# Kernel optimization log

Measured on AMD Instinct MI355X. Metric: run time of the kernel, lower is better.

Reference implementation:

```python
import jax, jax.numpy as jnp
import numpy as np

D_MODEL = 1024
N_HEADS = 16
D_K = D_MODEL // N_HEADS


def setup_inputs() -> dict:
    key = jax.random.key(0)
    ks = jax.random.split(key, 5)
    x = jax.random.normal(ks[0], (4, 2048, D_MODEL), dtype=jnp.float32)
    # nn.Linear stores weight as [out, in]; we store transposed [in, out] for x @ W
    w_qkv = jax.random.normal(ks[1], (D_MODEL, 3 * D_MODEL), dtype=jnp.float32) / np.sqrt(D_MODEL)
    b_qkv = jnp.zeros((3 * D_MODEL,), dtype=jnp.float32)
    w_fc = jax.random.normal(ks[2], (D_MODEL, D_MODEL), dtype=jnp.float32) / np.sqrt(D_MODEL)
    b_fc = jnp.zeros((D_MODEL,), dtype=jnp.float32)
    ln_g = jnp.ones((D_MODEL,), dtype=jnp.float32)
    ln_b = jnp.zeros((D_MODEL,), dtype=jnp.float32)
    return {"x": x, "w_qkv": w_qkv, "b_qkv": b_qkv, "w_fc": w_fc, "b_fc": b_fc,
            "ln_g": ln_g, "ln_b": ln_b}


def _layernorm(x, g, b, eps=1e-5):
    mu = jnp.mean(x, axis=-1, keepdims=True)
    var = jnp.mean(jnp.square(x - mu), axis=-1, keepdims=True)
    return (x - mu) * jax.lax.rsqrt(var + eps) * g + b


def reference(x, w_qkv, b_qkv, w_fc, b_fc, ln_g, ln_b):
    residual = x
    xn = _layernorm(x, ln_g, ln_b)
    B, L, D = xn.shape
    qkv = xn @ w_qkv + b_qkv  # [B, L, 3D]
    q, k, v = jnp.split(qkv, 3, axis=-1)
    # b l (h d) -> b h l d
    def to_heads(t):
        return t.reshape(B, L, N_HEADS, D_K).transpose(0, 2, 1, 3)
    q, k, v = to_heads(q), to_heads(k), to_heads(v)
    scale = 1.0 / np.sqrt(D_K)
    scores = jnp.einsum('bhld,bhmd->bhlm', q, k) * scale  # [B,H,L,L]
    attn = jax.nn.softmax(scores, axis=-1)
    # dropout is identity in eval mode
    out = jnp.einsum('bhlm,bhmd->bhld', attn, v)  # [B,H,L,d]
    out = out.transpose(0, 2, 1, 3).reshape(B, L, D)  # b h l d -> b l (h d)
    out = out @ w_fc + b_fc
    return out + residual
```

## Files before the change

kernel.cpp:

```cpp
#include <hip/hip_runtime.h>
#include <hip/hip_bf16.h>
#include <cstdint>
#include <cstddef>

using bf16 = __hip_bfloat16;
typedef __attribute__((ext_vector_type(4))) float f32x4;
typedef __attribute__((ext_vector_type(8))) short bf16x8;

#define D_MODEL 1024
#define SEQ     2048
#define NB      4
#define NHEAD   16
#define DHEAD   64
#define NROWS   (NB * SEQ)

__device__ __forceinline__ void load_lds16(const void* g, void* l) {
  __builtin_amdgcn_global_load_lds(
      (const __attribute__((address_space(1))) unsigned int*)g,
      (__attribute__((address_space(3))) unsigned int*)l, 16, 0, 0);
}

__device__ __forceinline__ unsigned short f2bf(float f) {
  bf16 h = __float2bfloat16(f);
  return *(unsigned short*)&h;
}

__device__ __forceinline__ unsigned pk_trunc(float a, float b) {
  union { float f; unsigned u; } ca, cb;
  ca.f = a; cb.f = b;
  return (ca.u >> 16) | (cb.u & 0xffff0000u);
}

__global__ __launch_bounds__(256) void prep_kernel(
    const float* __restrict__ x, const float* __restrict__ g,
    const float* __restrict__ bb, bf16* __restrict__ xn,
    const float* __restrict__ w_qkv, bf16* __restrict__ wqkvT,
    const float* __restrict__ w_fc, bf16* __restrict__ wfcT) {
  __shared__ float tile[32][33];
  if (blockIdx.x < 2048) {
    int row  = blockIdx.x * 4 + (threadIdx.x >> 6);
    int lane = threadIdx.x & 63;
    const float4* xr = (const float4*)(x + (size_t)row * D_MODEL);
    float v[16], s = 0.f;
#pragma unroll
    for (int i = 0; i < 4; i++) {
      float4 t = xr[lane + 64 * i];
      v[4 * i] = t.x; v[4 * i + 1] = t.y; v[4 * i + 2] = t.z; v[4 * i + 3] = t.w;
      s += t.x + t.y + t.z + t.w;
    }
#pragma unroll
    for (int off = 32; off; off >>= 1) s += __shfl_xor(s, off, 64);
    float mean = s * (1.f / D_MODEL);
    float vs = 0.f;
#pragma unroll
    for (int i = 0; i < 16; i++) { float d = v[i] - mean; vs += d * d; }
#pragma unroll
    for (int off = 32; off; off >>= 1) vs += __shfl_xor(vs, off, 64);
    float rstd = rsqrtf(vs * (1.f / D_MODEL) + 1e-5f);
    ushort4* op = (ushort4*)(xn + (size_t)row * D_MODEL);
#pragma unroll
    for (int i = 0; i < 4; i++) {
      float4 gv = ((const float4*)g)[lane + 64 * i];
      float4 bv = ((const float4*)bb)[lane + 64 * i];
      ushort4 o;
      o.x = f2bf((v[4 * i]     - mean) * rstd * gv.x + bv.x);
      o.y = f2bf((v[4 * i + 1] - mean) * rstd * gv.y + bv.y);
      o.z = f2bf((v[4 * i + 2] - mean) * rstd * gv.z + bv.z);
      o.w = f2bf((v[4 * i + 3] - mean) * rstd * gv.w + bv.w);
      op[lane + 64 * i] = o;
    }
  } else {
    int b2 = blockIdx.x - 2048;
    int bx = b2 & 127, by = b2 >> 7;
    const float* in; bf16* out; int C, c0;
    if (bx < 96) { in = w_qkv; out = wqkvT; C = 3072; c0 = bx * 32; }
    else         { in = w_fc;  out = wfcT;  C = 1024; c0 = (bx - 96) * 32; }
    int r0 = by * 32;
    int tx = threadIdx.x & 31, ty = threadIdx.x >> 5;
    for (int i = ty; i < 32; i += 8)
      tile[i][tx] = in[(size_t)(r0 + i) * C + c0 + tx];
    __syncthreads();
    for (int i = ty; i < 32; i += 8)
      out[(size_t)(c0 + i) * 1024 + r0 + tx] = __float2bfloat16(tile[tx][i]);
  }
}

__device__ __forceinline__ void store_ct(bf16* p, float v)  { *p = __float2bfloat16(v); }
__device__ __forceinline__ void store_ct(float* p, float v) { *p = v; }

template <int SPLIT, int RESID, typename CT>
__global__ __launch_bounds__(256) void gemm_bt(
    const bf16* __restrict__ A, const bf16* __restrict__ Bt,
    const float* __restrict__ bias, const float* __restrict__ resid,
    CT* __restrict__ C, bf16* __restrict__ vt, int M, int N, int K) {
  __shared__ __attribute__((aligned(16))) bf16 Alds[128 * 64];
  __shared__ __attribute__((aligned(16))) bf16 Blds[128 * 64];
  int tid = threadIdx.x, wave = tid >> 6, lane = tid & 63;
  int ntiles = N >> 7;
  int bm = blockIdx.x / ntiles, bn = blockIdx.x % ntiles;
  int m0 = bm << 7, n0 = bn << 7;
  int wm = (wave >> 1) << 6, wn = (wave & 1) << 6;
  int srow = tid >> 3;
  int sw8  = (((tid & 7) ^ (srow & 7)) << 3);
  int frow = lane & 15, quad = lane >> 4;
  const bf16* Ap[4];
  const bf16* Bp[4];
#pragma unroll
  for (int s = 0; s < 4; s++) {
    Ap[s] = A  + (size_t)(m0 + s * 32 + srow) * K + sw8;
    Bp[s] = Bt + (size_t)(n0 + s * 32 + srow) * K + sw8;
  }
  f32x4 acc[4][4] = {};
  for (int k0 = 0; k0 < K; k0 += 64) {
    __syncthreads();
#pragma unroll
    for (int s = 0; s < 4; s++) {
      load_lds16(Ap[s], (char*)Alds + s * 4096 + tid * 16);
      load_lds16(Bp[s], (char*)Blds + s * 4096 + tid * 16);
      Ap[s] += 64; Bp[s] += 64;
    }
    __syncthreads();
    bf16x8 af[4][2], bv[4][2];
#pragma unroll
    for (int i = 0; i < 4; i++)
#pragma unroll
      for (int kk = 0; kk < 2; kk++) {
        int e = (((kk * 4 + quad) ^ (frow & 7)) << 3);
        af[i][kk] = *(const bf16x8*)&Alds[(wm + i * 16 + frow) * 64 + e];
        bv[i][kk] = *(const bf16x8*)&Blds[(wn + i * 16 + frow) * 64 + e];
      }
#pragma unroll
    for (int i = 0; i < 4; i++)
#pragma unroll
      for (int j = 0; j < 4; j++) {
        acc[i][j] = __builtin_amdgcn_mfma_f32_16x16x32_bf16(af[i][0], bv[j][0], acc[i][j], 0, 0, 0);
        acc[i][j] = __builtin_amdgcn_mfma_f32_16x16x32_bf16(af[i][1], bv[j][1], acc[i][j], 0, 0, 0);
      }
  }
#pragma unroll
  for (int i = 0; i < 4; i++) {
    int row0 = m0 + wm + i * 16 + (quad << 2);
#pragma unroll
    for (int j = 0; j < 4; j++) {
      int col = n0 + wn + j * 16 + frow;
      float bvs = bias[col];
      if (SPLIT && col >= 2048) {
        int hd = col - 2048;
        int b = row0 >> 11, seq0 = row0 & 2047;
        int within = seq0 & 63, mt = within >> 4, q4 = (within >> 2) & 3;
        int pos = (seq0 & ~63) + ((mt >> 1) << 5) + (q4 << 3) + ((mt & 1) << 2);
        ushort4 pk;
        pk.x = f2bf(acc[i][j][0] + bvs);
        pk.y = f2bf(acc[i][j][1] + bvs);
        pk.z = f2bf(acc[i][j][2] + bvs);
        pk.w = f2bf(acc[i][j][3] + bvs);
        *(ushort4*)&vt[((size_t)(b * 1024 + hd)) * SEQ + pos] = pk;
      } else {
        int stride = SPLIT ? 2048 : N;
        float scale = (SPLIT && col < 1024) ? 0.18033688f : 1.0f;
#pragma unroll
        for (int r = 0; r < 4; r++) {
          size_t idx = (size_t)(row0 + r) * stride + col;
          float val = (acc[i][j][r] + bvs) * scale;
          if (RESID) val += resid[idx];
          store_ct(&C[idx], val);
        }
      }
    }
  }
}

__global__ __launch_bounds__(256) void gemm_fc64(
    const bf16* __restrict__ A, const bf16* __restrict__ Bt,
    const float* __restrict__ bias, const float* __restrict__ resid,
    float* __restrict__ out) {
  __shared__ __attribute__((aligned(16))) bf16 Alds[128 * 64];
  __shared__ __attribute__((aligned(16))) bf16 Blds[64 * 64];
  int tid = threadIdx.x, wave = tid >> 6, lane = tid & 63;
  int bm = blockIdx.x >> 4, bn = blockIdx.x & 15;
  int m0 = bm << 7, n0 = bn << 6;
  int wm = (wave >> 1) << 6, wn = (wave & 1) << 5;
  int srow = tid >> 3;
  int sw8  = (((tid & 7) ^ (srow & 7)) << 3);
  int frow = lane & 15, quad = lane >> 4;
  const bf16* Ap[4];
  const bf16* Bp[2];
#pragma unroll
  for (int s = 0; s < 4; s++)
    Ap[s] = A + (size_t)(m0 + s * 32 + srow) * 1024 + sw8;
#pragma unroll
  for (int s = 0; s < 2; s++)
    Bp[s] = Bt + (size_t)(n0 + s * 32 + srow) * 1024 + sw8;
  f32x4 acc[4][2] = {};
  for (int k0 = 0; k0 < 1024; k0 += 64) {
    __syncthreads();
#pragma unroll
    for (int s = 0; s < 4; s++) {
      load_lds16(Ap[s], (char*)Alds + s * 4096 + tid * 16);
      Ap[s] += 64;
    }
#pragma unroll
    for (int s = 0; s < 2; s++) {
      load_lds16(Bp[s], (char*)Blds + s * 4096 + tid * 16);
      Bp[s] += 64;
    }
    __syncthreads();
    bf16x8 af[4][2], bv[2][2];
#pragma unroll
    for (int kk = 0; kk < 2; kk++) {
      int e = (((kk * 4 + quad) ^ (frow & 7)) << 3);
#pragma unroll
      for (int i = 0; i < 4; i++)
        af[i][kk] = *(const bf16x8*)&Alds[(wm + i * 16 + frow) * 64 + e];
#pragma unroll
      for (int j = 0; j < 2; j++)
        bv[j][kk] = *(const bf16x8*)&Blds[(wn + j * 16 + frow) * 64 + e];
    }
#pragma unroll
    for (int i = 0; i < 4; i++)
#pragma unroll
      for (int j = 0; j < 2; j++) {
        acc[i][j] = __builtin_amdgcn_mfma_f32_16x16x32_bf16(af[i][0], bv[j][0], acc[i][j], 0, 0, 0);
        acc[i][j] = __builtin_amdgcn_mfma_f32_16x16x32_bf16(af[i][1], bv[j][1], acc[i][j], 0, 0, 0);
      }
  }
#pragma unroll
  for (int i = 0; i < 4; i++) {
    int row0 = m0 + wm + i * 16 + (quad << 2);
#pragma unroll
    for (int j = 0; j < 2; j++) {
      int col = n0 + wn + j * 16 + frow;
      float bvs = bias[col];
#pragma unroll
      for (int r = 0; r < 4; r++) {
        size_t idx = (size_t)(row0 + r) * 1024 + col;
        out[idx] = (acc[i][j][r] + bvs) + resid[idx];
      }
    }
  }
}


__device__ __forceinline__ void stage_kv(
    const bf16* Kp0, const bf16* Kp1, const bf16* Vp0, const bf16* Vp1,
    bf16* KB, bf16* VB, int tid) {
  load_lds16(Kp0, (char*)KB + tid * 16);
  load_lds16(Kp1, (char*)KB + 4096 + tid * 16);
  load_lds16(Vp0, (char*)VB + tid * 16);
  load_lds16(Vp1, (char*)VB + 4096 + tid * 16);
}

__device__ __forceinline__ void kv_tile(
    const bf16* KL, const bf16* VL, int frow, int e0,
    const bf16x8 (&qf)[2][2], f32x4 (&l4)[2], f32x4 (&o)[4][2]) {
  f32x4 s[4][2] = {};
#pragma unroll
  for (int mt = 0; mt < 4; mt++) {
    bf16x8 af0 = *(const bf16x8*)&KL[(mt * 16 + frow) * 64 + e0];
    bf16x8 af1 = *(const bf16x8*)&KL[(mt * 16 + frow) * 64 + (e0 ^ 32)];
#pragma unroll
    for (int qt2 = 0; qt2 < 2; qt2++) {
      s[mt][qt2] = __builtin_amdgcn_mfma_f32_16x16x32_bf16(af0, qf[qt2][0], s[mt][qt2], 0, 0, 0);
      s[mt][qt2] = __builtin_amdgcn_mfma_f32_16x16x32_bf16(af1, qf[qt2][1], s[mt][qt2], 0, 0, 0);
    }
  }
  uint2 pk[2][4];
#pragma unroll
  for (int qt2 = 0; qt2 < 2; qt2++)
#pragma unroll
    for (int mt = 0; mt < 4; mt++) {
      f32x4 pv;
      pv[0] = __builtin_amdgcn_exp2f(s[mt][qt2][0]);
      pv[1] = __builtin_amdgcn_exp2f(s[mt][qt2][1]);
      pv[2] = __builtin_amdgcn_exp2f(s[mt][qt2][2]);
      pv[3] = __builtin_amdgcn_exp2f(s[mt][qt2][3]);
      l4[qt2] += pv;
      pk[qt2][mt].x = pk_trunc(pv[0], pv[1]);
      pk[qt2][mt].y = pk_trunc(pv[2], pv[3]);
    }
#pragma unroll
  for (int dt = 0; dt < 4; dt++) {
    bf16x8 vf0 = *(const bf16x8*)&VL[(dt * 16 + frow) * 64 + e0];
    bf16x8 vf1 = *(const bf16x8*)&VL[(dt * 16 + frow) * 64 + (e0 ^ 32)];
#pragma unroll
    for (int qt2 = 0; qt2 < 2; qt2++) {
      union { unsigned u[4]; bf16x8 v; } pf0, pf1;
      pf0.u[0] = pk[qt2][0].x; pf0.u[1] = pk[qt2][0].y;
      pf0.u[2] = pk[qt2][1].x; pf0.u[3] = pk[qt2][1].y;
      pf1.u[0] = pk[qt2][2].x; pf1.u[1] = pk[qt2][2].y;
      pf1.u[2] = pk[qt2][3].x; pf1.u[3] = pk[qt2][3].y;
      o[dt][qt2] = __builtin_amdgcn_mfma_f32_16x16x32_bf16(vf0, pf0.v, o[dt][qt2], 0, 0, 0);
      o[dt][qt2] = __builtin_amdgcn_mfma_f32_16x16x32_bf16(vf1, pf1.v, o[dt][qt2], 0, 0, 0);
    }
  }
}

__global__ __launch_bounds__(256, 4) void attn_kernel(
    const bf16* __restrict__ qk, const bf16* __restrict__ vt,
    bf16* __restrict__ aout) {
  int bh = blockIdx.x;
  int qt = blockIdx.y;
  int bb = bh >> 4, h = bh & 15;
  const bf16* Qg = qk + (size_t)bb * SEQ * 2048 + h * DHEAD;
  const bf16* Kg = Qg + D_MODEL;
  const bf16* Vg = vt + (size_t)bh * DHEAD * SEQ;

  __shared__ __attribute__((aligned(16))) bf16 Qlds[128 * 64];
  __shared__ __attribute__((aligned(16))) bf16 Klds[64 * 64];
  __shared__ __attribute__((aligned(16))) bf16 Vlds[64 * 64];

  int tid = threadIdx.x, wave = tid >> 6, lane = tid & 63;
  int prow = tid >> 3, pch = tid & 7;
  int lch8 = ((pch ^ (prow & 7)) << 3);
  int frow = lane & 15, quad = lane >> 4;
  int e0 = ((quad ^ (frow & 7)) << 3);
  int q0 = qt * 128;

  bf16* K0 = Klds;  bf16* V0 = Vlds;
  bf16* K1 = Qlds;  bf16* V1 = Qlds + 64 * 64;

  const bf16* Kp0 = Kg + (size_t)prow * 2048 + lch8;
  const bf16* Kp1 = Kg + (size_t)(32 + prow) * 2048 + lch8;
  const bf16* Vp0 = Vg + (size_t)prow * SEQ + lch8;
  const bf16* Vp1 = Vg + (size_t)(32 + prow) * SEQ + lch8;
  const size_t KT = (size_t)1 << 17;

#pragma unroll
  for (int s2 = 0; s2 < 4; s2++)
    load_lds16(Qg + (size_t)(q0 + s2 * 32 + prow) * 2048 + lch8,
               (char*)Qlds + s2 * 4096 + tid * 16);
  __syncthreads();
  bf16x8 qf[2][2];
#pragma unroll
  for (int qt2 = 0; qt2 < 2; qt2++)
#pragma unroll
    for (int kk = 0; kk < 2; kk++)
      qf[qt2][kk] =
          *(const bf16x8*)&Qlds[(wave * 32 + qt2 * 16 + frow) * 64 + (e0 ^ (kk * 32))];
  stage_kv(Kp0, Kp1, Vp0, Vp1, K0, V0, tid);
  __syncthreads();

  f32x4 l4[2] = {};
  f32x4 o[4][2] = {};

#pragma unroll 1
  for (int kt = 0; kt < 30; kt += 2) {
    stage_kv(Kp0 + KT, Kp1 + KT, Vp0 + 64, Vp1 + 64, K1, V1, tid);
    kv_tile(K0, V0, frow, e0, qf, l4, o);
    __syncthreads();
    stage_kv(Kp0 + 2 * KT, Kp1 + 2 * KT, Vp0 + 128, Vp1 + 128, K0, V0, tid);
    kv_tile(K1, V1, frow, e0, qf, l4, o);
    __syncthreads();
    Kp0 += 2 * KT; Kp1 += 2 * KT; Vp0 += 128; Vp1 += 128;
  }
  stage_kv(Kp0 + KT, Kp1 + KT, Vp0 + 64, Vp1 + 64, K1, V1, tid);
  kv_tile(K0, V0, frow, e0, qf, l4, o);
  __syncthreads();
  kv_tile(K1, V1, frow, e0, qf, l4, o);

  float linv[2];
#pragma unroll
  for (int qt2 = 0; qt2 < 2; qt2++) {
    float v = (l4[qt2][0] + l4[qt2][1]) + (l4[qt2][2] + l4[qt2][3]);
    v += __shfl_xor(v, 16, 64);
    v += __shfl_xor(v, 32, 64);
    linv[qt2] = 1.f / v;
  }

  __syncthreads();
  bf16* Tw = (wave == 0) ? Qlds
           : (wave == 1) ? Qlds + 32 * 80
           : (wave == 2) ? Klds : Vlds;
#pragma unroll
  for (int qt2 = 0; qt2 < 2; qt2++)
#pragma unroll
    for (int dt = 0; dt < 4; dt++) {
      ushort4 pk;
      pk.x = f2bf(o[dt][qt2][0] * linv[qt2]);
      pk.y = f2bf(o[dt][qt2][1] * linv[qt2]);
      pk.z = f2bf(o[dt][qt2][2] * linv[qt2]);
      pk.w = f2bf(o[dt][qt2][3] * linv[qt2]);
      *(ushort4*)&Tw[(qt2 * 16 + frow) * 80 + dt * 16 + quad * 4] = pk;
    }
  int rq = lane >> 1, d0 = (lane & 1) * 32;
  size_t grow = (size_t)(bb * SEQ + q0 + wave * 32 + rq);
#pragma unroll
  for (int i = 0; i < 4; i++) {
    bf16x8 v8 = *(const bf16x8*)&Tw[rq * 80 + d0 + i * 8];
    *(bf16x8*)&aout[grow * D_MODEL + h * DHEAD + d0 + i * 8] = v8;
  }
}

extern "C" void kernel_launch(void* const* d_in, const int* in_sizes, int n_in,
                              void* d_out, int out_size, void* d_ws, size_t ws_size,
                              hipStream_t stream) {
  const float* x     = (const float*)d_in[0];
  const float* w_qkv = (const float*)d_in[1];
  const float* b_qkv = (const float*)d_in[2];
  const float* w_fc  = (const float*)d_in[3];
  const float* b_fc  = (const float*)d_in[4];
  const float* ln_g  = (const float*)d_in[5];
  const float* ln_b  = (const float*)d_in[6];
  float* out = (float*)d_out;

  char* ws = (char*)d_ws;
  bf16* xn    = (bf16*)(ws);
  bf16* wqkvT = (bf16*)(ws + (16u << 20));
  bf16* wfcT  = (bf16*)(ws + (22u << 20));
  bf16* qk    = (bf16*)(ws + (24u << 20));
  bf16* vt    = (bf16*)(ws + (56u << 20));
  bf16* aout  = (bf16*)(ws);

  prep_kernel<<<2048 + 4096, 256, 0, stream>>>(
      x, ln_g, ln_b, xn, w_qkv, wqkvT, w_fc, wfcT);
  gemm_bt<1, 0, bf16><<<(NROWS / 128) * (3 * D_MODEL / 128), 256, 0, stream>>>(
      xn, wqkvT, b_qkv, nullptr, qk, vt, NROWS, 3 * D_MODEL, D_MODEL);
  attn_kernel<<<dim3(NB * NHEAD, SEQ / 128), 256, 0, stream>>>(qk, vt, aout);
  gemm_fc64<<<1024, 256, 0, stream>>>(aout, wfcT, b_fc, x, out);
}
```

Baseline: 265.1 us.

## Fuse all stages into one persistent cooperative kernel with grid syncs

Merges the LayerNorm/weight-transpose prep, QKV GEMM, attention and output projection into a single cooperative kernel of 1024 blocks. Grid-wide barriers separate the stages, and shared memory is reused through one 32KB buffer. The aim is to remove three kernel launch gaps and their tail effects; it also adds s_setprio around the attention MFMA sections. In exchange, every stage is forced to the same occupancy (launch bounds 4, one shared LDS size) and grid.sync costs are added, with a fallback to separate kernels if the cooperative launch fails.

```diff
diff --git a/kernel.cpp b/kernel.cpp
--- a/kernel.cpp
+++ b/kernel.cpp
@@ -1,7 +1,10 @@
 #include <hip/hip_runtime.h>
+#include <hip/hip_cooperative_groups.h>
 #include <hip/hip_bf16.h>
 #include <cstdint>
 #include <cstddef>
+
+namespace cg = cooperative_groups;
 
 using bf16 = __hip_bfloat16;
 typedef __attribute__((ext_vector_type(4))) float f32x4;
@@ -31,21 +34,20 @@
   return (ca.u >> 16) | (cb.u & 0xffff0000u);
 }
 
-__global__ __launch_bounds__(256) void prep_kernel(
-    const float* __restrict__ x, const float* __restrict__ g,
+__device__ __forceinline__ void stage_prep(
+    int v, char* smem, const float* __restrict__ x, const float* __restrict__ g,
     const float* __restrict__ bb, bf16* __restrict__ xn,
     const float* __restrict__ w_qkv, bf16* __restrict__ wqkvT,
     const float* __restrict__ w_fc, bf16* __restrict__ wfcT) {
-  __shared__ float tile[32][33];
-  if (blockIdx.x < 2048) {
-    int row  = blockIdx.x * 4 + (threadIdx.x >> 6);
+  if (v < 2048) {
+    int row  = v * 4 + (threadIdx.x >> 6);
     int lane = threadIdx.x & 63;
     const float4* xr = (const float4*)(x + (size_t)row * D_MODEL);
-    float v[16], s = 0.f;
+    float vv[16], s = 0.f;
 #pragma unroll
     for (int i = 0; i < 4; i++) {
       float4 t = xr[lane + 64 * i];
-      v[4 * i] = t.x; v[4 * i + 1] = t.y; v[4 * i + 2] = t.z; v[4 * i + 3] = t.w;
+      vv[4 * i] = t.x; vv[4 * i + 1] = t.y; vv[4 * i + 2] = t.z; vv[4 * i + 3] = t.w;
       s += t.x + t.y + t.z + t.w;
     }
 #pragma unroll
@@ -53,7 +55,7 @@
     float mean = s * (1.f / D_MODEL);
     float vs = 0.f;
 #pragma unroll
-    for (int i = 0; i < 16; i++) { float d = v[i] - mean; vs += d * d; }
+    for (int i = 0; i < 16; i++) { float d = vv[i] - mean; vs += d * d; }
 #pragma unroll
     for (int off = 32; off; off >>= 1) vs += __shfl_xor(vs, off, 64);
     float rstd = rsqrtf(vs * (1.f / D_MODEL) + 1e-5f);
@@ -63,14 +65,15 @@
       float4 gv = ((const float4*)g)[lane + 64 * i];
       float4 bv = ((const float4*)bb)[lane + 64 * i];
       ushort4 o;
-      o.x = f2bf((v[4 * i]     - mean) * rstd * gv.x + bv.x);
-      o.y = f2bf((v[4 * i + 1] - mean) * rstd * gv.y + bv.y);
-      o.z = f2bf((v[4 * i + 2] - mean) * rstd * gv.z + bv.z);
-      o.w = f2bf((v[4 * i + 3] - mean) * rstd * gv.w + bv.w);
+      o.x = f2bf((vv[4 * i]     - mean) * rstd * gv.x + bv.x);
+      o.y = f2bf((vv[4 * i + 1] - mean) * rstd * gv.y + bv.y);
+      o.z = f2bf((vv[4 * i + 2] - mean) * rstd * gv.z + bv.z);
+      o.w = f2bf((vv[4 * i + 3] - mean) * rstd * gv.w + bv.w);
       op[lane + 64 * i] = o;
     }
   } else {
-    int b2 = blockIdx.x - 2048;
+    float (*tile)[33] = (float(*)[33])smem;
+    int b2 = v - 2048;
     int bx = b2 & 127, by = b2 >> 7;
     const float* in; bf16* out; int C, c0;
     if (bx < 96) { in = w_qkv; out = wqkvT; C = 3072; c0 = bx * 32; }
@@ -85,19 +88,13 @@
   }
 }
 
-__device__ __forceinline__ void store_ct(bf16* p, float v)  { *p = __float2bfloat16(v); }
-__device__ __forceinline__ void store_ct(float* p, float v) { *p = v; }
-
-template <int SPLIT, int RESID, typename CT>
-__global__ __launch_bounds__(256) void gemm_bt(
-    const bf16* __restrict__ A, const bf16* __restrict__ Bt,
-    const float* __restrict__ bias, const float* __restrict__ resid,
-    CT* __restrict__ C, bf16* __restrict__ vt, int M, int N, int K) {
-  __shared__ __attribute__((aligned(16))) bf16 Alds[128 * 64];
-  __shared__ __attribute__((aligned(16))) bf16 Blds[128 * 64];
+__device__ __forceinline__ void stage_qkv(
+    int v, char* smem, const bf16* __restrict__ A, const bf16* __restrict__ Bt,
+    const float* __restrict__ bias, bf16* __restrict__ C, bf16* __restrict__ vt) {
+  bf16* Alds = (bf16*)smem;
+  bf16* Blds = (bf16*)(smem + 16384);
   int tid = threadIdx.x, wave = tid >> 6, lane = tid & 63;
-  int ntiles = N >> 7;
-  int bm = blockIdx.x / ntiles, bn = blockIdx.x % ntiles;
+  int bm = v / 24, bn = v % 24;
   int m0 = bm << 7, n0 = bn << 7;
   int wm = (wave >> 1) << 6, wn = (wave & 1) << 6;
   int srow = tid >> 3;
@@ -107,11 +104,11 @@
   const bf16* Bp[4];
 #pragma unroll
   for (int s = 0; s < 4; s++) {
-    Ap[s] = A  + (size_t)(m0 + s * 32 + srow) * K + sw8;
-    Bp[s] = Bt + (size_t)(n0 + s * 32 + srow) * K + sw8;
+    Ap[s] = A  + (size_t)(m0 + s * 32 + srow) * 1024 + sw8;
+    Bp[s] = Bt + (size_t)(n0 + s * 32 + srow) * 1024 + sw8;
   }
   f32x4 acc[4][4] = {};
-  for (int k0 = 0; k0 < K; k0 += 64) {
+  for (int k0 = 0; k0 < 1024; k0 += 64) {
     __syncthreads();
 #pragma unroll
     for (int s = 0; s < 4; s++) {
@@ -144,7 +141,7 @@
     for (int j = 0; j < 4; j++) {
       int col = n0 + wn + j * 16 + frow;
       float bvs = bias[col];
-      if (SPLIT && col >= 2048) {
+      if (col >= 2048) {
         int hd = col - 2048;
         int b = row0 >> 11, seq0 = row0 & 2047;
         int within = seq0 & 63, mt = within >> 4, q4 = (within >> 2) & 3;
@@ -156,90 +153,16 @@
         pk.w = f2bf(acc[i][j][3] + bvs);
         *(ushort4*)&vt[((size_t)(b * 1024 + hd)) * SEQ + pos] = pk;
       } else {
-        int stride = SPLIT ? 2048 : N;
-        float scale = (SPLIT && col < 1024) ? 0.18033688f : 1.0f;
+        float scale = (col < 1024) ? 0.18033688f : 1.0f;
 #pragma unroll
         for (int r = 0; r < 4; r++) {
-          size_t idx = (size_t)(row0 + r) * stride + col;
-          float val = (acc[i][j][r] + bvs) * scale;
-          if (RESID) val += resid[idx];
-          store_ct(&C[idx], val);
+          size_t idx = (size_t)(row0 + r) * 2048 + col;
+          C[idx] = __float2bfloat16((acc[i][j][r] + bvs) * scale);
         }
       }
     }
   }
 }
-
-__global__ __launch_bounds__(256) void gemm_fc64(
-    const bf16* __restrict__ A, const bf16* __restrict__ Bt,
-    const float* __restrict__ bias, const float* __restrict__ resid,
-    float* __restrict__ out) {
-  __shared__ __attribute__((aligned(16))) bf16 Alds[128 * 64];
-  __shared__ __attribute__((aligned(16))) bf16 Blds[64 * 64];
-  int tid = threadIdx.x, wave = tid >> 6, lane = tid & 63;
-  int bm = blockIdx.x >> 4, bn = blockIdx.x & 15;
-  int m0 = bm << 7, n0 = bn << 6;
-  int wm = (wave >> 1) << 6, wn = (wave & 1) << 5;
-  int srow = tid >> 3;
-  int sw8  = (((tid & 7) ^ (srow & 7)) << 3);
-  int frow = lane & 15, quad = lane >> 4;
-  const bf16* Ap[4];
-  const bf16* Bp[2];
-#pragma unroll
-  for (int s = 0; s < 4; s++)
-    Ap[s] = A + (size_t)(m0 + s * 32 + srow) * 1024 + sw8;
-#pragma unroll
-  for (int s = 0; s < 2; s++)
-    Bp[s] = Bt + (size_t)(n0 + s * 32 + srow) * 1024 + sw8;
-  f32x4 acc[4][2] = {};
-  for (int k0 = 0; k0 < 1024; k0 += 64) {
-    __syncthreads();
-#pragma unroll
-    for (int s = 0; s < 4; s++) {
-      load_lds16(Ap[s], (char*)Alds + s * 4096 + tid * 16);
-      Ap[s] += 64;
-    }
-#pragma unroll
-    for (int s = 0; s < 2; s++) {
-      load_lds16(Bp[s], (char*)Blds + s * 4096 + tid * 16);
-      Bp[s] += 64;
-    }
-    __syncthreads();
-    bf16x8 af[4][2], bv[2][2];
-#pragma unroll
-    for (int kk = 0; kk < 2; kk++) {
-      int e = (((kk * 4 + quad) ^ (frow & 7)) << 3);
-#pragma unroll
-      for (int i = 0; i < 4; i++)
-        af[i][kk] = *(const bf16x8*)&Alds[(wm + i * 16 + frow) * 64 + e];
-#pragma unroll
-      for (int j = 0; j < 2; j++)
-        bv[j][kk] = *(const bf16x8*)&Blds[(wn + j * 16 + frow) * 64 + e];
-    }
-#pragma unroll
-    for (int i = 0; i < 4; i++)
-#pragma unroll
-      for (int j = 0; j < 2; j++) {
-        acc[i][j] = __builtin_amdgcn_mfma_f32_16x16x32_bf16(af[i][0], bv[j][0], acc[i][j], 0, 0, 0);
-        acc[i][j] = __builtin_amdgcn_mfma_f32_16x16x32_bf16(af[i][1], bv[j][1], acc[i][j], 0, 0, 0);
-      }
-  }
-#pragma unroll
-  for (int i = 0; i < 4; i++) {
-    int row0 = m0 + wm + i * 16 + (quad << 2);
-#pragma unroll
-    for (int j = 0; j < 2; j++) {
-      int col = n0 + wn + j * 16 + frow;
-      float bvs = bias[col];
-#pragma unroll
-      for (int r = 0; r < 4; r++) {
-        size_t idx = (size_t)(row0 + r) * 1024 + col;
-        out[idx] = (acc[i][j][r] + bvs) + resid[idx];
-      }
-    }
-  }
-}
-
 
 __device__ __forceinline__ void stage_kv(
     const bf16* Kp0, const bf16* Kp1, const bf16* Vp0, const bf16* Vp1,
@@ -254,6 +177,7 @@
     const bf16* KL, const bf16* VL, int frow, int e0,
     const bf16x8 (&qf)[2][2], f32x4 (&l4)[2], f32x4 (&o)[4][2]) {
   f32x4 s[4][2] = {};
+  __builtin_amdgcn_s_setprio(1);
 #pragma unroll
   for (int mt = 0; mt < 4; mt++) {
     bf16x8 af0 = *(const bf16x8*)&KL[(mt * 16 + frow) * 64 + e0];
@@ -264,6 +188,7 @@
       s[mt][qt2] = __builtin_amdgcn_mfma_f32_16x16x32_bf16(af1, qf[qt2][1], s[mt][qt2], 0, 0, 0);
     }
   }
+  __builtin_amdgcn_s_setprio(0);
   uint2 pk[2][4];
 #pragma unroll
   for (int qt2 = 0; qt2 < 2; qt2++)
@@ -278,6 +203,7 @@
       pk[qt2][mt].x = pk_trunc(pv[0], pv[1]);
       pk[qt2][mt].y = pk_trunc(pv[2], pv[3]);
     }
+  __builtin_amdgcn_s_setprio(1);
 #pragma unroll
   for (int dt = 0; dt < 4; dt++) {
     bf16x8 vf0 = *(const bf16x8*)&VL[(dt * 16 + frow) * 64 + e0];
@@ -293,21 +219,22 @@
       o[dt][qt2] = __builtin_amdgcn_mfma_f32_16x16x32_bf16(vf1, pf1.v, o[dt][qt2], 0, 0, 0);
     }
   }
-}
-
-__global__ __launch_bounds__(256, 4) void attn_kernel(
-    const bf16* __restrict__ qk, const bf16* __restrict__ vt,
+  __builtin_amdgcn_s_setprio(0);
+}
+
+__device__ __forceinline__ void stage_attn(
+    int v, char* smem, const bf16* __restrict__ qk, const bf16* __restrict__ vt,
     bf16* __restrict__ aout) {
-  int bh = blockIdx.x;
-  int qt = blockIdx.y;
+  int bh = v & 63;
+  int qt = v >> 6;
   int bb = bh >> 4, h = bh & 15;
   const bf16* Qg = qk + (size_t)bb * SEQ * 2048 + h * DHEAD;
   const bf16* Kg = Qg + D_MODEL;
   const bf16* Vg = vt + (size_t)bh * DHEAD * SEQ;
 
-  __shared__ __attribute__((aligned(16))) bf16 Qlds[128 * 64];
-  __shared__ __attribute__((aligned(16))) bf16 Klds[64 * 64];
-  __shared__ __attribute__((aligned(16))) bf16 Vlds[64 * 64];
+  bf16* Qlds = (bf16*)smem;
+  bf16* Klds = (bf16*)(smem + 16384);
+  bf16* Vlds = (bf16*)(smem + 24576);
 
   int tid = threadIdx.x, wave = tid >> 6, lane = tid & 63;
   int prow = tid >> 3, pch = tid & 7;
@@ -361,10 +288,10 @@
   float linv[2];
 #pragma unroll
   for (int qt2 = 0; qt2 < 2; qt2++) {
-    float v = (l4[qt2][0] + l4[qt2][1]) + (l4[qt2][2] + l4[qt2][3]);
-    v += __shfl_xor(v, 16, 64);
-    v += __shfl_xor(v, 32, 64);
-    linv[qt2] = 1.f / v;
+    float w = (l4[qt2][0] + l4[qt2][1]) + (l4[qt2][2] + l4[qt2][3]);
+    w += __shfl_xor(w, 16, 64);
+    w += __shfl_xor(w, 32, 64);
+    linv[qt2] = 1.f / w;
   }
 
   __syncthreads();
@@ -389,6 +316,130 @@
     bf16x8 v8 = *(const bf16x8*)&Tw[rq * 80 + d0 + i * 8];
     *(bf16x8*)&aout[grow * D_MODEL + h * DHEAD + d0 + i * 8] = v8;
   }
+}
+
+__device__ __forceinline__ void stage_fc(
+    int v, char* smem, const bf16* __restrict__ A, const bf16* __restrict__ Bt,
+    const float* __restrict__ bias, const float* __restrict__ resid,
+    float* __restrict__ out) {
+  bf16* Alds = (bf16*)smem;
+  bf16* Blds = (bf16*)(smem + 16384);
+  int tid = threadIdx.x, wave = tid >> 6, lane = tid & 63;
+  int bm = v >> 4, bn = v & 15;
+  int m0 = bm << 7, n0 = bn << 6;
+  int wm = (wave >> 1) << 6, wn = (wave & 1) << 5;
+  int srow = tid >> 3;
+  int sw8  = (((tid & 7) ^ (srow & 7)) << 3);
+  int frow = lane & 15, quad = lane >> 4;
+  const bf16* Ap[4];
+  const bf16* Bp[2];
+#pragma unroll
+  for (int s = 0; s < 4; s++)
+    Ap[s] = A + (size_t)(m0 + s * 32 + srow) * 1024 + sw8;
+#pragma unroll
+  for (int s = 0; s < 2; s++)
+    Bp[s] = Bt + (size_t)(n0 + s * 32 + srow) * 1024 + sw8;
+  f32x4 acc[4][2] = {};
+  for (int k0 = 0; k0 < 1024; k0 += 64) {
+    __syncthreads();
+#pragma unroll
+    for (int s = 0; s < 4; s++) {
+      load_lds16(Ap[s], (char*)Alds + s * 4096 + tid * 16);
+      Ap[s] += 64;
+    }
+#pragma unroll
+    for (int s = 0; s < 2; s++) {
+      load_lds16(Bp[s], (char*)Blds + s * 4096 + tid * 16);
+      Bp[s] += 64;
+    }
+    __syncthreads();
+    bf16x8 af[4][2], bv[2][2];
+#pragma unroll
+    for (int kk = 0; kk < 2; kk++) {
+      int e = (((kk * 4 + quad) ^ (frow & 7)) << 3);
+#pragma unroll
+      for (int i = 0; i < 4; i++)
+        af[i][kk] = *(const bf16x8*)&Alds[(wm + i * 16 + frow) * 64 + e];
+#pragma unroll
+      for (int j = 0; j < 2; j++)
+        bv[j][kk] = *(const bf16x8*)&Blds[(wn + j * 16 + frow) * 64 + e];
+    }
+#pragma unroll
+    for (int i = 0; i < 4; i++)
+#pragma unroll
+      for (int j = 0; j < 2; j++) {
+        acc[i][j] = __builtin_amdgcn_mfma_f32_16x16x32_bf16(af[i][0], bv[j][0], acc[i][j], 0, 0, 0);
+        acc[i][j] = __builtin_amdgcn_mfma_f32_16x16x32_bf16(af[i][1], bv[j][1], acc[i][j], 0, 0, 0);
+      }
+  }
+#pragma unroll
+  for (int i = 0; i < 4; i++) {
+    int row0 = m0 + wm + i * 16 + (quad << 2);
+#pragma unroll
+    for (int j = 0; j < 2; j++) {
+      int col = n0 + wn + j * 16 + frow;
+      float bvs = bias[col];
+#pragma unroll
+      for (int r = 0; r < 4; r++) {
+        size_t idx = (size_t)(row0 + r) * 1024 + col;
+        out[idx] = (acc[i][j][r] + bvs) + resid[idx];
+      }
+    }
+  }
+}
+
+__global__ void __launch_bounds__(256, 4) fused_all(
+    const float* x, const float* ln_g, const float* ln_b,
+    const float* w_qkv, const float* b_qkv,
+    const float* w_fc, const float* b_fc,
+    bf16* xn, bf16* wqkvT, bf16* wfcT, bf16* qk, bf16* vt, bf16* aout,
+    float* out) {
+  __shared__ __attribute__((aligned(16))) char smem[32768];
+  cg::grid_group grid = cg::this_grid();
+  int bid = blockIdx.x;
+
+#pragma unroll 1
+  for (int v = bid; v < 6144; v += 1024) {
+    stage_prep(v, smem, x, ln_g, ln_b, xn, w_qkv, wqkvT, w_fc, wfcT);
+    __syncthreads();
+  }
+  grid.sync();
+#pragma unroll 1
+  for (int v = bid; v < 1536; v += 1024) {
+    stage_qkv(v, smem, xn, wqkvT, b_qkv, qk, vt);
+    __syncthreads();
+  }
+  grid.sync();
+  stage_attn(bid, smem, qk, vt, aout);
+  grid.sync();
+  stage_fc(bid, smem, aout, wfcT, b_fc, x, out);
+}
+
+__global__ void __launch_bounds__(256, 4) prep_kernel_s(
+    const float* __restrict__ x, const float* __restrict__ g,
+    const float* __restrict__ bb, bf16* __restrict__ xn,
+    const float* __restrict__ w_qkv, bf16* __restrict__ wqkvT,
+    const float* __restrict__ w_fc, bf16* __restrict__ wfcT) {
+  __shared__ __attribute__((aligned(16))) char smem[32768];
+  stage_prep(blockIdx.x, smem, x, g, bb, xn, w_qkv, wqkvT, w_fc, wfcT);
+}
+__global__ void __launch_bounds__(256, 4) qkv_kernel_s(
+    const bf16* __restrict__ A, const bf16* __restrict__ Bt,
+    const float* __restrict__ bias, bf16* __restrict__ C, bf16* __restrict__ vt) {
+  __shared__ __attribute__((aligned(16))) char smem[32768];
+  stage_qkv(blockIdx.x, smem, A, Bt, bias, C, vt);
+}
+__global__ void __launch_bounds__(256, 4) attn_kernel_s(
+    const bf16* __restrict__ qk, const bf16* __restrict__ vt, bf16* __restrict__ aout) {
+  __shared__ __attribute__((aligned(16))) char smem[32768];
+  stage_attn(blockIdx.x, smem, qk, vt, aout);
+}
+__global__ void __launch_bounds__(256, 4) fc_kernel_s(
+    const bf16* __restrict__ A, const bf16* __restrict__ Bt,
+    const float* __restrict__ bias, const float* __restrict__ resid,
+    float* __restrict__ out) {
+  __shared__ __attribute__((aligned(16))) char smem[32768];
+  stage_fc(blockIdx.x, smem, A, Bt, bias, resid, out);
 }
 
 extern "C" void kernel_launch(void* const* d_in, const int* in_sizes, int n_in,
@@ -411,10 +462,16 @@
   bf16* vt    = (bf16*)(ws + (56u << 20));
   bf16* aout  = (bf16*)(ws);
 
-  prep_kernel<<<2048 + 4096, 256, 0, stream>>>(
-      x, ln_g, ln_b, xn, w_qkv, wqkvT, w_fc, wfcT);
-  gemm_bt<1, 0, bf16><<<(NROWS / 128) * (3 * D_MODEL / 128), 256, 0, stream>>>(
-      xn, wqkvT, b_qkv, nullptr, qk, vt, NROWS, 3 * D_MODEL, D_MODEL);
-  attn_kernel<<<dim3(NB * NHEAD, SEQ / 128), 256, 0, stream>>>(qk, vt, aout);
-  gemm_fc64<<<1024, 256, 0, stream>>>(aout, wfcT, b_fc, x, out);
-}
+  void* kargs[] = {
+      (void*)&x, (void*)&ln_g, (void*)&ln_b, (void*)&w_qkv, (void*)&b_qkv,
+      (void*)&w_fc, (void*)&b_fc, (void*)&xn, (void*)&wqkvT, (void*)&wfcT,
+      (void*)&qk, (void*)&vt, (void*)&aout, (void*)&out};
+  hipError_t err = hipLaunchCooperativeKernel(
+      reinterpret_cast<void*>(fused_all), dim3(1024), dim3(256), kargs, 0, stream);
+  if (err != hipSuccess) {
+    prep_kernel_s<<<6144, 256, 0, stream>>>(x, ln_g, ln_b, xn, w_qkv, wqkvT, w_fc, wfcT);
+    qkv_kernel_s<<<1536, 256, 0, stream>>>(xn, wqkvT, b_qkv, qk, vt);
+    attn_kernel_s<<<1024, 256, 0, stream>>>(qk, vt, aout);
+    fc_kernel_s<<<1024, 256, 0, stream>>>(aout, wfcT, b_fc, x, out);
+  }
+}
```

Result: slower. 783.1 us (+195.4%).
